# Kernel optimization log

Hardware: AMD Instinct MI355X
Metric: run time of the kernel (lower is better)

Reference implementation:

```python
import jax, jax.numpy as jnp
import numpy as np

# torch.rrelu in eval mode uses slope = (lower+upper)/2 = (1/8 + 1/3)/2
RRELU_SLOPE = (1.0 / 8.0 + 1.0 / 3.0) / 2.0

N_NODES = 50000
N_EDGES = 800000
EMB_FEATS = 128
IN_FEATS = 128
HIDDEN = 64


def setup_inputs() -> dict:
    key = jax.random.key(0)
    ks = jax.random.split(key, 16)
    z = jax.random.normal(ks[0], (N_NODES, EMB_FEATS), dtype=jnp.float32)
    x = jax.random.normal(ks[1], (N_NODES, IN_FEATS), dtype=jnp.float32)
    edge_index = jax.random.randint(ks[2], (2, N_EDGES), 0, N_NODES, dtype=jnp.int32)

    def glorot(k, shape):
        fan_in, fan_out = shape
        lim = jnp.sqrt(6.0 / (fan_in + fan_out))
        return jax.random.uniform(k, shape, jnp.float32, -lim, lim)

    return {
        "z": z,
        "x": x,
        "edge_index": edge_index,
        "W_e1": glorot(ks[3], (EMB_FEATS, HIDDEN)),
        "b_e1": jnp.zeros((HIDDEN,), jnp.float32),
        "W_e2": glorot(ks[4], (HIDDEN, HIDDEN)),
        "b_e2": jnp.zeros((HIDDEN,), jnp.float32),
        "W_f1": glorot(ks[5], (IN_FEATS, HIDDEN)),
        "b_f1": jnp.zeros((HIDDEN,), jnp.float32),
        "W_f2": glorot(ks[6], (HIDDEN, HIDDEN)),
        "b_f2": jnp.zeros((HIDDEN,), jnp.float32),
        "W_out": glorot(ks[7], (HIDDEN, 1)),
        "b_out": jnp.zeros((1,), jnp.float32),
    }


def gcn_conv(h_in, W, b, src, dst, n_nodes):
    """PyG GCNConv: self-loops + symmetric deg^-1/2 normalization."""
    h = h_in @ W  # [N, out]
    # degree of self-loop-augmented graph: indeg + 1
    indeg = jax.ops.segment_sum(
        jnp.ones(dst.shape[0], h.dtype), dst, num_segments=n_nodes)
    deg = indeg + 1.0
    dinv = jnp.where(deg > 0, 1.0 / jnp.sqrt(deg), 0.0)  # [N]
    norm = dinv[src] * dinv[dst]  # [E]
    # neighbor messages (gather + scatter-add)
    agg = jax.ops.segment_sum(h[src] * norm[:, None], dst, num_segments=n_nodes)
    # self-loop contribution: dinv[i]*dinv[i]*h[i]
    agg = agg + h * (dinv * dinv)[:, None]
    return agg + b


def _rrelu(t):
    return jnp.where(t >= 0, t, t * RRELU_SLOPE)


def reference(z, x, edge_index, W_e1, b_e1, W_e2, b_e2,
              W_f1, b_f1, W_f2, b_f2, W_out, b_out):
    src, dst = edge_index[0], edge_index[1]
    n = z.shape[0]
    ze = _rrelu(gcn_conv(z, W_e1, b_e1, src, dst, n))
    ze = jnp.tanh(gcn_conv(ze, W_e2, b_e2, src, dst, n))
    xf = _rrelu(gcn_conv(x, W_f1, b_f1, src, dst, n))
    xf = jnp.tanh(gcn_conv(xf, W_f2, b_f2, src, dst, n))
    return (ze * xf) @ W_out + b_out  # [N, 1]
```

## Files before the change

### kernel.cpp

```cpp
#include <hip/hip_runtime.h>
#include <hip/hip_fp16.h>
#include <math.h>

#define RRELU_SLOPE 0.22916667f


__global__ __launch_bounds__(256) void k_deg(const int* __restrict__ dst, int E,
                                             int* __restrict__ cnt) {
    int e = blockIdx.x * 256 + threadIdx.x;
    if (e < E) atomicAdd(&cnt[dst[e]], 1);
}

__global__ __launch_bounds__(256) void k_scan1(const int* __restrict__ cnt, int N,
                                               int* __restrict__ bsum) {
    int i = blockIdx.x * 256 + threadIdx.x;
    int v = (i < N) ? cnt[i] : 0;
    for (int o = 32; o >= 1; o >>= 1) v += __shfl_xor(v, o, 64);
    __shared__ int ws[4];
    if ((threadIdx.x & 63) == 0) ws[threadIdx.x >> 6] = v;
    __syncthreads();
    if (threadIdx.x == 0) bsum[blockIdx.x] = ws[0] + ws[1] + ws[2] + ws[3];
}

__global__ __launch_bounds__(256) void k_scan2(const int* __restrict__ bsum, int NB,
                                               int* __restrict__ boff,
                                               int* __restrict__ rowp, int N, int E) {
    __shared__ int s[256];
    int t = threadIdx.x;
    int v[4];
    int loc = 0;
    for (int i = 0; i < 4; i++) {
        int idx = t * 4 + i;
        v[i] = (idx < NB) ? bsum[idx] : 0;
        loc += v[i];
    }
    s[t] = loc;
    __syncthreads();
    for (int o = 1; o < 256; o <<= 1) {
        int u = (t >= o) ? s[t - o] : 0;
        __syncthreads();
        s[t] += u;
        __syncthreads();
    }
    int excl = s[t] - loc;
    for (int i = 0; i < 4; i++) {
        int idx = t * 4 + i;
        if (idx < NB) { boff[idx] = excl; excl += v[i]; }
    }
    if (t == 0) rowp[N] = E;
}

__global__ __launch_bounds__(256) void k_scan3(const int* __restrict__ cnt,
                                               const int* __restrict__ boff, int N,
                                               int* __restrict__ rowp,
                                               int* __restrict__ nxt,
                                               float* __restrict__ dinv) {
    int i = blockIdx.x * 256 + threadIdx.x;
    int lane = threadIdx.x & 63, wid = threadIdx.x >> 6;
    int v = (i < N) ? cnt[i] : 0;
    int inc = v;
    for (int o = 1; o < 64; o <<= 1) {
        int u = __shfl_up(inc, o, 64);
        if (lane >= o) inc += u;
    }
    __shared__ int wsum[4];
    if (lane == 63) wsum[wid] = inc;
    __syncthreads();
    int wo = 0;
    for (int w = 0; w < wid; w++) wo += wsum[w];
    if (i < N) {
        int excl = inc - v + wo + boff[blockIdx.x];
        rowp[i] = excl;
        nxt[i] = excl;
        dinv[i] = 1.0f / sqrtf((float)v + 1.0f);
    }
}

__global__ __launch_bounds__(256) void k_fill(const int* __restrict__ src,
                                              const int* __restrict__ dst, int E,
                                              int* __restrict__ nxt,
                                              const float* __restrict__ dinv,
                                              int2* __restrict__ pair) {
    int e = blockIdx.x * 256 + threadIdx.x;
    if (e >= E) return;
    int s = src[e], d = dst[e];
    int p = atomicAdd(&nxt[d], 1);
    float v = dinv[s] * dinv[d];
    pair[p] = make_int2(s, __float_as_int(v));
}

__global__ __launch_bounds__(256) void k_mm1(const float* __restrict__ Zin,
                                             const float* __restrict__ Xin,
                                             const float* __restrict__ Wz,
                                             const float* __restrict__ Wx,
                                             __half2* __restrict__ H, int N) {
    __shared__ float Asz[64][20], Asx[64][20];
    __shared__ float Wsz[16][64], Wsx[16][64];
    const int tid = threadIdx.x;
    const int tc = tid & 15, tr = tid >> 4;
    const int row0 = blockIdx.x * 64;
    const int srow = tid >> 2, sk = (tid & 3) * 4;
    const int wk = tid >> 4, wc = (tid & 15) * 4;

    float cz[4][4] = {}, cx[4][4] = {};

    for (int k0 = 0; k0 < 128; k0 += 16) {
        float4 a0 = make_float4(0.f, 0.f, 0.f, 0.f);
        float4 a1 = make_float4(0.f, 0.f, 0.f, 0.f);
        int gr = row0 + srow;
        if (gr < N) {
            a0 = *(const float4*)(Zin + (size_t)gr * 128 + k0 + sk);
            a1 = *(const float4*)(Xin + (size_t)gr * 128 + k0 + sk);
        }
        float4 w0 = *(const float4*)(Wz + (size_t)(k0 + wk) * 64 + wc);
        float4 w1 = *(const float4*)(Wx + (size_t)(k0 + wk) * 64 + wc);
        __syncthreads();
        *(float4*)&Asz[srow][sk] = a0;
        *(float4*)&Asx[srow][sk] = a1;
        *(float4*)&Wsz[wk][wc] = w0;
        *(float4*)&Wsx[wk][wc] = w1;
        __syncthreads();

#pragma unroll
        for (int k = 0; k < 16; k += 4) {
            float4 vz[4], vx[4];
#pragma unroll
            for (int i = 0; i < 4; i++) {
                vz[i] = *(const float4*)&Asz[tr * 4 + i][k];
                vx[i] = *(const float4*)&Asx[tr * 4 + i][k];
            }
#pragma unroll
            for (int kk = 0; kk < 4; kk++) {
                float4 wzv = *(const float4*)&Wsz[k + kk][tc * 4];
                float4 wxv = *(const float4*)&Wsx[k + kk][tc * 4];
#pragma unroll
                for (int i = 0; i < 4; i++) {
                    float a = ((const float*)&vz[i])[kk];
                    float b = ((const float*)&vx[i])[kk];
                    cz[i][0] = fmaf(a, wzv.x, cz[i][0]);
                    cz[i][1] = fmaf(a, wzv.y, cz[i][1]);
                    cz[i][2] = fmaf(a, wzv.z, cz[i][2]);
                    cz[i][3] = fmaf(a, wzv.w, cz[i][3]);
                    cx[i][0] = fmaf(b, wxv.x, cx[i][0]);
                    cx[i][1] = fmaf(b, wxv.y, cx[i][1]);
                    cx[i][2] = fmaf(b, wxv.z, cx[i][2]);
                    cx[i][3] = fmaf(b, wxv.w, cx[i][3]);
                }
            }
        }
    }

#pragma unroll
    for (int i = 0; i < 4; i++) {
        int r = row0 + tr * 4 + i;
        if (r < N) {
            union { __half2 h[4]; float4 f; } u;
#pragma unroll
            for (int j = 0; j < 4; j++) u.h[j] = __floats2half2_rn(cz[i][j], cx[i][j]);
            *(float4*)(H + (size_t)r * 64 + tc * 4) = u.f;
        }
    }
}

__global__ __launch_bounds__(256) void k_mm2i(const float* __restrict__ Azx,
                                              const float* __restrict__ Wz,
                                              const float* __restrict__ Wx,
                                              __half2* __restrict__ H, int N) {
    __shared__ float As[64][36];
    __shared__ float Wsz[16][64], Wsx[16][64];
    const int tid = threadIdx.x;
    const int tc = tid & 15, tr = tid >> 4;
    const int row0 = blockIdx.x * 64;
    const int srow = tid >> 2, soff = (tid & 3) * 8;
    const int wk = tid >> 4, wc = (tid & 15) * 4;

    float cz[4][4] = {}, cx[4][4] = {};

    for (int k0 = 0; k0 < 64; k0 += 16) {
        float4 a0 = make_float4(0.f, 0.f, 0.f, 0.f);
        float4 a1 = make_float4(0.f, 0.f, 0.f, 0.f);
        int gr = row0 + srow;
        if (gr < N) {
            a0 = *(const float4*)(Azx + (size_t)gr * 128 + 2 * k0 + soff);
            a1 = *(const float4*)(Azx + (size_t)gr * 128 + 2 * k0 + soff + 4);
        }
        float4 w0 = *(const float4*)(Wz + (size_t)(k0 + wk) * 64 + wc);
        float4 w1 = *(const float4*)(Wx + (size_t)(k0 + wk) * 64 + wc);
        __syncthreads();
        *(float4*)&As[srow][soff] = a0;
        *(float4*)&As[srow][soff + 4] = a1;
        *(float4*)&Wsz[wk][wc] = w0;
        *(float4*)&Wsx[wk][wc] = w1;
        __syncthreads();

#pragma unroll
        for (int k = 0; k < 16; k += 2) {
            float4 v[4];
#pragma unroll
            for (int i = 0; i < 4; i++) v[i] = *(const float4*)&As[tr * 4 + i][2 * k];
#pragma unroll
            for (int kk = 0; kk < 2; kk++) {
                float4 wzv = *(const float4*)&Wsz[k + kk][tc * 4];
                float4 wxv = *(const float4*)&Wsx[k + kk][tc * 4];
#pragma unroll
                for (int i = 0; i < 4; i++) {
                    float a = kk ? v[i].z : v[i].x;
                    float b = kk ? v[i].w : v[i].y;
                    cz[i][0] = fmaf(a, wzv.x, cz[i][0]);
                    cz[i][1] = fmaf(a, wzv.y, cz[i][1]);
                    cz[i][2] = fmaf(a, wzv.z, cz[i][2]);
                    cz[i][3] = fmaf(a, wzv.w, cz[i][3]);
                    cx[i][0] = fmaf(b, wxv.x, cx[i][0]);
                    cx[i][1] = fmaf(b, wxv.y, cx[i][1]);
                    cx[i][2] = fmaf(b, wxv.z, cx[i][2]);
                    cx[i][3] = fmaf(b, wxv.w, cx[i][3]);
                }
            }
        }
    }

#pragma unroll
    for (int i = 0; i < 4; i++) {
        int r = row0 + tr * 4 + i;
        if (r < N) {
            union { __half2 h[4]; float4 f; } u;
#pragma unroll
            for (int j = 0; j < 4; j++) u.h[j] = __floats2half2_rn(cz[i][j], cx[i][j]);
            *(float4*)(H + (size_t)r * 64 + tc * 4) = u.f;
        }
    }
}

__global__ __launch_bounds__(256) void k_agg_act(
    const int* __restrict__ rowp, const int2* __restrict__ pair,
    const float* __restrict__ dinv, const __half2* __restrict__ H,
    const float* __restrict__ bz, const float* __restrict__ bx,
    float* __restrict__ A, int N) {
    int wid = threadIdx.x >> 6, lane = threadIdx.x & 63;
    int i = blockIdx.x * 4 + wid;
    if (i >= N) return;
    int beg = rowp[i], end = rowp[i + 1];
    float2 s0 = {0.f, 0.f}, s1 = {0.f, 0.f}, s2 = {0.f, 0.f}, s3 = {0.f, 0.f};
    int p = beg;
    if (p < end && (p & 1)) {
        int2 cv = pair[p++];
        float2 h = __half22float2(H[(size_t)cv.x * 64 + lane]);
        float w = __int_as_float(cv.y);
        s0.x = fmaf(w, h.x, s0.x);
        s0.y = fmaf(w, h.y, s0.y);
    }
    for (; p + 8 <= end; p += 8) {
        int4 pa = *(const int4*)(pair + p);
        int4 pb = *(const int4*)(pair + p + 2);
        int4 pc = *(const int4*)(pair + p + 4);
        int4 pd = *(const int4*)(pair + p + 6);
        float2 h0 = __half22float2(H[(size_t)pa.x * 64 + lane]);
        float2 h1 = __half22float2(H[(size_t)pa.z * 64 + lane]);
        float2 h2 = __half22float2(H[(size_t)pb.x * 64 + lane]);
        float2 h3 = __half22float2(H[(size_t)pb.z * 64 + lane]);
        float2 h4 = __half22float2(H[(size_t)pc.x * 64 + lane]);
        float2 h5 = __half22float2(H[(size_t)pc.z * 64 + lane]);
        float2 h6 = __half22float2(H[(size_t)pd.x * 64 + lane]);
        float2 h7 = __half22float2(H[(size_t)pd.z * 64 + lane]);
        float w0 = __int_as_float(pa.y), w1 = __int_as_float(pa.w);
        float w2 = __int_as_float(pb.y), w3 = __int_as_float(pb.w);
        float w4 = __int_as_float(pc.y), w5 = __int_as_float(pc.w);
        float w6 = __int_as_float(pd.y), w7 = __int_as_float(pd.w);
        s0.x = fmaf(w0, h0.x, s0.x); s0.y = fmaf(w0, h0.y, s0.y);
        s1.x = fmaf(w1, h1.x, s1.x); s1.y = fmaf(w1, h1.y, s1.y);
        s2.x = fmaf(w2, h2.x, s2.x); s2.y = fmaf(w2, h2.y, s2.y);
        s3.x = fmaf(w3, h3.x, s3.x); s3.y = fmaf(w3, h3.y, s3.y);
        s0.x = fmaf(w4, h4.x, s0.x); s0.y = fmaf(w4, h4.y, s0.y);
        s1.x = fmaf(w5, h5.x, s1.x); s1.y = fmaf(w5, h5.y, s1.y);
        s2.x = fmaf(w6, h6.x, s2.x); s2.y = fmaf(w6, h6.y, s2.y);
        s3.x = fmaf(w7, h7.x, s3.x); s3.y = fmaf(w7, h7.y, s3.y);
    }
    for (; p + 2 <= end; p += 2) {
        int4 pa = *(const int4*)(pair + p);
        float2 h0 = __half22float2(H[(size_t)pa.x * 64 + lane]);
        float2 h1 = __half22float2(H[(size_t)pa.z * 64 + lane]);
        float w0 = __int_as_float(pa.y), w1 = __int_as_float(pa.w);
        s0.x = fmaf(w0, h0.x, s0.x); s0.y = fmaf(w0, h0.y, s0.y);
        s1.x = fmaf(w1, h1.x, s1.x); s1.y = fmaf(w1, h1.y, s1.y);
    }
    if (p < end) {
        int2 cv = pair[p];
        float2 h = __half22float2(H[(size_t)cv.x * 64 + lane]);
        float w = __int_as_float(cv.y);
        s0.x = fmaf(w, h.x, s0.x);
        s0.y = fmaf(w, h.y, s0.y);
    }
    float sz = (s0.x + s1.x) + (s2.x + s3.x);
    float sx = (s0.y + s1.y) + (s2.y + s3.y);
    float dv = dinv[i], sw = dv * dv;
    float2 hs = __half22float2(H[(size_t)i * 64 + lane]);
    sz = fmaf(sw, hs.x, sz) + bz[lane];
    sx = fmaf(sw, hs.y, sx) + bx[lane];
    sz = sz >= 0.f ? sz : sz * RRELU_SLOPE;
    sx = sx >= 0.f ? sx : sx * RRELU_SLOPE;
    *((float2*)(A + (size_t)i * 128) + lane) = make_float2(sz, sx);
}

__global__ __launch_bounds__(256) void k_agg_final(
    const int* __restrict__ rowp, const int2* __restrict__ pair,
    const float* __restrict__ dinv, const __half2* __restrict__ H,
    const float* __restrict__ bz, const float* __restrict__ bx,
    const float* __restrict__ Wout, const float* __restrict__ bout,
    float* __restrict__ out, int N) {
    int wid = threadIdx.x >> 6, lane = threadIdx.x & 63;
    int i = blockIdx.x * 4 + wid;
    if (i >= N) return;
    int beg = rowp[i], end = rowp[i + 1];
    float2 s0 = {0.f, 0.f}, s1 = {0.f, 0.f}, s2 = {0.f, 0.f}, s3 = {0.f, 0.f};
    int p = beg;
    if (p < end && (p & 1)) {
        int2 cv = pair[p++];
        float2 h = __half22float2(H[(size_t)cv.x * 64 + lane]);
        float w = __int_as_float(cv.y);
        s0.x = fmaf(w, h.x, s0.x);
        s0.y = fmaf(w, h.y, s0.y);
    }
    for (; p + 8 <= end; p += 8) {
        int4 pa = *(const int4*)(pair + p);
        int4 pb = *(const int4*)(pair + p + 2);
        int4 pc = *(const int4*)(pair + p + 4);
        int4 pd = *(const int4*)(pair + p + 6);
        float2 h0 = __half22float2(H[(size_t)pa.x * 64 + lane]);
        float2 h1 = __half22float2(H[(size_t)pa.z * 64 + lane]);
        float2 h2 = __half22float2(H[(size_t)pb.x * 64 + lane]);
        float2 h3 = __half22float2(H[(size_t)pb.z * 64 + lane]);
        float2 h4 = __half22float2(H[(size_t)pc.x * 64 + lane]);
        float2 h5 = __half22float2(H[(size_t)pc.z * 64 + lane]);
        float2 h6 = __half22float2(H[(size_t)pd.x * 64 + lane]);
        float2 h7 = __half22float2(H[(size_t)pd.z * 64 + lane]);
        float w0 = __int_as_float(pa.y), w1 = __int_as_float(pa.w);
        float w2 = __int_as_float(pb.y), w3 = __int_as_float(pb.w);
        float w4 = __int_as_float(pc.y), w5 = __int_as_float(pc.w);
        float w6 = __int_as_float(pd.y), w7 = __int_as_float(pd.w);
        s0.x = fmaf(w0, h0.x, s0.x); s0.y = fmaf(w0, h0.y, s0.y);
        s1.x = fmaf(w1, h1.x, s1.x); s1.y = fmaf(w1, h1.y, s1.y);
        s2.x = fmaf(w2, h2.x, s2.x); s2.y = fmaf(w2, h2.y, s2.y);
        s3.x = fmaf(w3, h3.x, s3.x); s3.y = fmaf(w3, h3.y, s3.y);
        s0.x = fmaf(w4, h4.x, s0.x); s0.y = fmaf(w4, h4.y, s0.y);
        s1.x = fmaf(w5, h5.x, s1.x); s1.y = fmaf(w5, h5.y, s1.y);
        s2.x = fmaf(w6, h6.x, s2.x); s2.y = fmaf(w6, h6.y, s2.y);
        s3.x = fmaf(w7, h7.x, s3.x); s3.y = fmaf(w7, h7.y, s3.y);
    }
    for (; p + 2 <= end; p += 2) {
        int4 pa = *(const int4*)(pair + p);
        float2 h0 = __half22float2(H[(size_t)pa.x * 64 + lane]);
        float2 h1 = __half22float2(H[(size_t)pa.z * 64 + lane]);
        float w0 = __int_as_float(pa.y), w1 = __int_as_float(pa.w);
        s0.x = fmaf(w0, h0.x, s0.x); s0.y = fmaf(w0, h0.y, s0.y);
        s1.x = fmaf(w1, h1.x, s1.x); s1.y = fmaf(w1, h1.y, s1.y);
    }
    if (p < end) {
        int2 cv = pair[p];
        float2 h = __half22float2(H[(size_t)cv.x * 64 + lane]);
        float w = __int_as_float(cv.y);
        s0.x = fmaf(w, h.x, s0.x);
        s0.y = fmaf(w, h.y, s0.y);
    }
    float sz = (s0.x + s1.x) + (s2.x + s3.x);
    float sx = (s0.y + s1.y) + (s2.y + s3.y);
    float dv = dinv[i], sw = dv * dv;
    float2 hs = __half22float2(H[(size_t)i * 64 + lane]);
    sz = fmaf(sw, hs.x, sz) + bz[lane];
    sx = fmaf(sw, hs.y, sx) + bx[lane];
    float prod = tanhf(sz) * tanhf(sx) * Wout[lane];
    for (int o = 32; o >= 1; o >>= 1) prod += __shfl_xor(prod, o, 64);
    if (lane == 0) out[i] = prod + bout[0];
}


extern "C" void kernel_launch(void* const* d_in, const int* in_sizes, int n_in,
                              void* d_out, int out_size, void* d_ws, size_t ws_size,
                              hipStream_t stream) {
    const float* z = (const float*)d_in[0];
    const float* x = (const float*)d_in[1];
    const int* ei = (const int*)d_in[2];
    const float* We1 = (const float*)d_in[3];
    const float* be1 = (const float*)d_in[4];
    const float* We2 = (const float*)d_in[5];
    const float* be2 = (const float*)d_in[6];
    const float* Wf1 = (const float*)d_in[7];
    const float* bf1 = (const float*)d_in[8];
    const float* Wf2 = (const float*)d_in[9];
    const float* bf2 = (const float*)d_in[10];
    const float* Wout = (const float*)d_in[11];
    const float* bout = (const float*)d_in[12];
    float* out = (float*)d_out;

    int N = in_sizes[0] / 128;
    int E = in_sizes[2] / 2;
    const int* src = ei;
    const int* dst = ei + E;

    char* base = (char*)d_ws;
    size_t off = 0;
    auto take = [&](size_t nbytes) -> char* {
        char* p = base + off;
        off = (off + nbytes + 255) & ~(size_t)255;
        return p;
    };
    int NB = (N + 255) / 256;
    int* cnt = (int*)take((size_t)N * 4);
    int* bsum = (int*)take(1024 * 4);
    int* boff = (int*)take(1024 * 4);
    int* rowp = (int*)take(((size_t)N + 1) * 4);
    int* nxt = (int*)take((size_t)N * 4);
    float* dinv = (float*)take((size_t)N * 4);
    int2* pair = (int2*)take((size_t)E * 8);
    __half2* hzx = (__half2*)take((size_t)N * 64 * 4);
    float* azx = (float*)take((size_t)N * 128 * 4);

    hipMemsetAsync(cnt, 0, (size_t)N * 4, stream);

    int egrid = (E + 255) / 256;
    k_deg<<<egrid, 256, 0, stream>>>(dst, E, cnt);
    k_scan1<<<NB, 256, 0, stream>>>(cnt, N, bsum);
    k_scan2<<<1, 256, 0, stream>>>(bsum, NB, boff, rowp, N, E);
    k_scan3<<<NB, 256, 0, stream>>>(cnt, boff, N, rowp, nxt, dinv);
    k_fill<<<egrid, 256, 0, stream>>>(src, dst, E, nxt, dinv, pair);

    int mmgrid = (N + 63) / 64;
    int agrid = (N + 3) / 4;

    k_mm1<<<mmgrid, 256, 0, stream>>>(z, x, We1, Wf1, hzx, N);
    k_agg_act<<<agrid, 256, 0, stream>>>(rowp, pair, dinv, hzx, be1, bf1, azx, N);
    k_mm2i<<<mmgrid, 256, 0, stream>>>(azx, We2, Wf2, hzx, N);
    k_agg_final<<<agrid, 256, 0, stream>>>(rowp, pair, dinv, hzx, be2, bf2, Wout,
                                           bout, out, N);
}
```

Before: 227.2 us.

## Build CSR from atomic ranks and recompute edge weights from dinv in aggregation

The degree-count kernel now records each edge's atomic rank, so the fill kernel places source indices directly at rowp[dst]+rank with no second atomic pass. The CSR stores only source indices (4 bytes per edge) instead of (src, weight) pairs, and the aggregation kernels recompute each edge weight as dinv[src]*dinv[dst] on the fly. This removes the second round of atomics and halves edge-list traffic in both aggregation passes. In exchange it adds a per-edge rank array and an extra random dinv gather per edge in each aggregation.

```diff
diff --git a/kernel.cpp b/kernel.cpp
--- a/kernel.cpp
+++ b/kernel.cpp
@@ -6,9 +6,10 @@
 
 
 __global__ __launch_bounds__(256) void k_deg(const int* __restrict__ dst, int E,
-                                             int* __restrict__ cnt) {
+                                             int* __restrict__ cnt,
+                                             int* __restrict__ rank) {
     int e = blockIdx.x * 256 + threadIdx.x;
-    if (e < E) atomicAdd(&cnt[dst[e]], 1);
+    if (e < E) rank[e] = atomicAdd(&cnt[dst[e]], 1);
 }
 
 __global__ __launch_bounds__(256) void k_scan1(const int* __restrict__ cnt, int N,
@@ -53,7 +54,6 @@
 __global__ __launch_bounds__(256) void k_scan3(const int* __restrict__ cnt,
                                                const int* __restrict__ boff, int N,
                                                int* __restrict__ rowp,
-                                               int* __restrict__ nxt,
                                                float* __restrict__ dinv) {
     int i = blockIdx.x * 256 + threadIdx.x;
     int lane = threadIdx.x & 63, wid = threadIdx.x >> 6;
@@ -71,22 +71,19 @@
     if (i < N) {
         int excl = inc - v + wo + boff[blockIdx.x];
         rowp[i] = excl;
-        nxt[i] = excl;
         dinv[i] = 1.0f / sqrtf((float)v + 1.0f);
     }
 }
 
 __global__ __launch_bounds__(256) void k_fill(const int* __restrict__ src,
-                                              const int* __restrict__ dst, int E,
-                                              int* __restrict__ nxt,
-                                              const float* __restrict__ dinv,
-                                              int2* __restrict__ pair) {
+                                              const int* __restrict__ dst,
+                                              const int* __restrict__ rank, int E,
+                                              const int* __restrict__ rowp,
+                                              int* __restrict__ csrc) {
     int e = blockIdx.x * 256 + threadIdx.x;
     if (e >= E) return;
-    int s = src[e], d = dst[e];
-    int p = atomicAdd(&nxt[d], 1);
-    float v = dinv[s] * dinv[d];
-    pair[p] = make_int2(s, __float_as_int(v));
+    int d = dst[e];
+    csrc[rowp[d] + rank[e]] = src[e];
 }
 
 __global__ __launch_bounds__(256) void k_mm1(const float* __restrict__ Zin,
@@ -231,8 +228,16 @@
     }
 }
 
+#define AGG_EDGE(S, C)                                            \
+    {                                                             \
+        float2 h_ = __half22float2(H[(size_t)(C)*64 + lane]);     \
+        float w_ = dinv[C] * dvi;                                 \
+        S.x = fmaf(w_, h_.x, S.x);                                \
+        S.y = fmaf(w_, h_.y, S.y);                                \
+    }
+
 __global__ __launch_bounds__(256) void k_agg_act(
-    const int* __restrict__ rowp, const int2* __restrict__ pair,
+    const int* __restrict__ rowp, const int* __restrict__ csrc,
     const float* __restrict__ dinv, const __half2* __restrict__ H,
     const float* __restrict__ bz, const float* __restrict__ bx,
     float* __restrict__ A, int N) {
@@ -240,59 +245,40 @@
     int i = blockIdx.x * 4 + wid;
     if (i >= N) return;
     int beg = rowp[i], end = rowp[i + 1];
+    float dvi = dinv[i];
     float2 s0 = {0.f, 0.f}, s1 = {0.f, 0.f}, s2 = {0.f, 0.f}, s3 = {0.f, 0.f};
     int p = beg;
-    if (p < end && (p & 1)) {
-        int2 cv = pair[p++];
-        float2 h = __half22float2(H[(size_t)cv.x * 64 + lane]);
-        float w = __int_as_float(cv.y);
-        s0.x = fmaf(w, h.x, s0.x);
-        s0.y = fmaf(w, h.y, s0.y);
+    while (p < end && (p & 3)) {
+        int c = csrc[p++];
+        AGG_EDGE(s0, c);
     }
     for (; p + 8 <= end; p += 8) {
-        int4 pa = *(const int4*)(pair + p);
-        int4 pb = *(const int4*)(pair + p + 2);
-        int4 pc = *(const int4*)(pair + p + 4);
-        int4 pd = *(const int4*)(pair + p + 6);
-        float2 h0 = __half22float2(H[(size_t)pa.x * 64 + lane]);
-        float2 h1 = __half22float2(H[(size_t)pa.z * 64 + lane]);
-        float2 h2 = __half22float2(H[(size_t)pb.x * 64 + lane]);
-        float2 h3 = __half22float2(H[(size_t)pb.z * 64 + lane]);
-        float2 h4 = __half22float2(H[(size_t)pc.x * 64 + lane]);
-        float2 h5 = __half22float2(H[(size_t)pc.z * 64 + lane]);
-        float2 h6 = __half22float2(H[(size_t)pd.x * 64 + lane]);
-        float2 h7 = __half22float2(H[(size_t)pd.z * 64 + lane]);
-        float w0 = __int_as_float(pa.y), w1 = __int_as_float(pa.w);
-        float w2 = __int_as_float(pb.y), w3 = __int_as_float(pb.w);
-        float w4 = __int_as_float(pc.y), w5 = __int_as_float(pc.w);
-        float w6 = __int_as_float(pd.y), w7 = __int_as_float(pd.w);
-        s0.x = fmaf(w0, h0.x, s0.x); s0.y = fmaf(w0, h0.y, s0.y);
-        s1.x = fmaf(w1, h1.x, s1.x); s1.y = fmaf(w1, h1.y, s1.y);
-        s2.x = fmaf(w2, h2.x, s2.x); s2.y = fmaf(w2, h2.y, s2.y);
-        s3.x = fmaf(w3, h3.x, s3.x); s3.y = fmaf(w3, h3.y, s3.y);
-        s0.x = fmaf(w4, h4.x, s0.x); s0.y = fmaf(w4, h4.y, s0.y);
-        s1.x = fmaf(w5, h5.x, s1.x); s1.y = fmaf(w5, h5.y, s1.y);
-        s2.x = fmaf(w6, h6.x, s2.x); s2.y = fmaf(w6, h6.y, s2.y);
-        s3.x = fmaf(w7, h7.x, s3.x); s3.y = fmaf(w7, h7.y, s3.y);
-    }
-    for (; p + 2 <= end; p += 2) {
-        int4 pa = *(const int4*)(pair + p);
-        float2 h0 = __half22float2(H[(size_t)pa.x * 64 + lane]);
-        float2 h1 = __half22float2(H[(size_t)pa.z * 64 + lane]);
-        float w0 = __int_as_float(pa.y), w1 = __int_as_float(pa.w);
-        s0.x = fmaf(w0, h0.x, s0.x); s0.y = fmaf(w0, h0.y, s0.y);
-        s1.x = fmaf(w1, h1.x, s1.x); s1.y = fmaf(w1, h1.y, s1.y);
-    }
-    if (p < end) {
-        int2 cv = pair[p];
-        float2 h = __half22float2(H[(size_t)cv.x * 64 + lane]);
-        float w = __int_as_float(cv.y);
-        s0.x = fmaf(w, h.x, s0.x);
-        s0.y = fmaf(w, h.y, s0.y);
+        int4 ca = *(const int4*)(csrc + p);
+        int4 cb = *(const int4*)(csrc + p + 4);
+        AGG_EDGE(s0, ca.x);
+        AGG_EDGE(s1, ca.y);
+        AGG_EDGE(s2, ca.z);
+        AGG_EDGE(s3, ca.w);
+        AGG_EDGE(s0, cb.x);
+        AGG_EDGE(s1, cb.y);
+        AGG_EDGE(s2, cb.z);
+        AGG_EDGE(s3, cb.w);
+    }
+    if (p + 4 <= end) {
+        int4 ca = *(const int4*)(csrc + p);
+        AGG_EDGE(s0, ca.x);
+        AGG_EDGE(s1, ca.y);
+        AGG_EDGE(s2, ca.z);
+        AGG_EDGE(s3, ca.w);
+        p += 4;
+    }
+    while (p < end) {
+        int c = csrc[p++];
+        AGG_EDGE(s0, c);
     }
     float sz = (s0.x + s1.x) + (s2.x + s3.x);
     float sx = (s0.y + s1.y) + (s2.y + s3.y);
-    float dv = dinv[i], sw = dv * dv;
+    float sw = dvi * dvi;
     float2 hs = __half22float2(H[(size_t)i * 64 + lane]);
     sz = fmaf(sw, hs.x, sz) + bz[lane];
     sx = fmaf(sw, hs.y, sx) + bx[lane];
@@ -302,7 +288,7 @@
 }
 
 __global__ __launch_bounds__(256) void k_agg_final(
-    const int* __restrict__ rowp, const int2* __restrict__ pair,
+    const int* __restrict__ rowp, const int* __restrict__ csrc,
     const float* __restrict__ dinv, const __half2* __restrict__ H,
     const float* __restrict__ bz, const float* __restrict__ bx,
     const float* __restrict__ Wout, const float* __restrict__ bout,
@@ -311,59 +297,40 @@
     int i = blockIdx.x * 4 + wid;
     if (i >= N) return;
     int beg = rowp[i], end = rowp[i + 1];
+    float dvi = dinv[i];
     float2 s0 = {0.f, 0.f}, s1 = {0.f, 0.f}, s2 = {0.f, 0.f}, s3 = {0.f, 0.f};
     int p = beg;
-    if (p < end && (p & 1)) {
-        int2 cv = pair[p++];
-        float2 h = __half22float2(H[(size_t)cv.x * 64 + lane]);
-        float w = __int_as_float(cv.y);
-        s0.x = fmaf(w, h.x, s0.x);
-        s0.y = fmaf(w, h.y, s0.y);
+    while (p < end && (p & 3)) {
+        int c = csrc[p++];
+        AGG_EDGE(s0, c);
     }
     for (; p + 8 <= end; p += 8) {
-        int4 pa = *(const int4*)(pair + p);
-        int4 pb = *(const int4*)(pair + p + 2);
-        int4 pc = *(const int4*)(pair + p + 4);
-        int4 pd = *(const int4*)(pair + p + 6);
-        float2 h0 = __half22float2(H[(size_t)pa.x * 64 + lane]);
-        float2 h1 = __half22float2(H[(size_t)pa.z * 64 + lane]);
-        float2 h2 = __half22float2(H[(size_t)pb.x * 64 + lane]);
-        float2 h3 = __half22float2(H[(size_t)pb.z * 64 + lane]);
-        float2 h4 = __half22float2(H[(size_t)pc.x * 64 + lane]);
-        float2 h5 = __half22float2(H[(size_t)pc.z * 64 + lane]);
-        float2 h6 = __half22float2(H[(size_t)pd.x * 64 + lane]);
-        float2 h7 = __half22float2(H[(size_t)pd.z * 64 + lane]);
-        float w0 = __int_as_float(pa.y), w1 = __int_as_float(pa.w);
-        float w2 = __int_as_float(pb.y), w3 = __int_as_float(pb.w);
-        float w4 = __int_as_float(pc.y), w5 = __int_as_float(pc.w);
-        float w6 = __int_as_float(pd.y), w7 = __int_as_float(pd.w);
-        s0.x = fmaf(w0, h0.x, s0.x); s0.y = fmaf(w0, h0.y, s0.y);
-        s1.x = fmaf(w1, h1.x, s1.x); s1.y = fmaf(w1, h1.y, s1.y);
-        s2.x = fmaf(w2, h2.x, s2.x); s2.y = fmaf(w2, h2.y, s2.y);
-        s3.x = fmaf(w3, h3.x, s3.x); s3.y = fmaf(w3, h3.y, s3.y);
-        s0.x = fmaf(w4, h4.x, s0.x); s0.y = fmaf(w4, h4.y, s0.y);
-        s1.x = fmaf(w5, h5.x, s1.x); s1.y = fmaf(w5, h5.y, s1.y);
-        s2.x = fmaf(w6, h6.x, s2.x); s2.y = fmaf(w6, h6.y, s2.y);
-        s3.x = fmaf(w7, h7.x, s3.x); s3.y = fmaf(w7, h7.y, s3.y);
-    }
-    for (; p + 2 <= end; p += 2) {
-        int4 pa = *(const int4*)(pair + p);
-        float2 h0 = __half22float2(H[(size_t)pa.x * 64 + lane]);
-        float2 h1 = __half22float2(H[(size_t)pa.z * 64 + lane]);
-        float w0 = __int_as_float(pa.y), w1 = __int_as_float(pa.w);
-        s0.x = fmaf(w0, h0.x, s0.x); s0.y = fmaf(w0, h0.y, s0.y);
-        s1.x = fmaf(w1, h1.x, s1.x); s1.y = fmaf(w1, h1.y, s1.y);
-    }
-    if (p < end) {
-        int2 cv = pair[p];
-        float2 h = __half22float2(H[(size_t)cv.x * 64 + lane]);
-        float w = __int_as_float(cv.y);
-        s0.x = fmaf(w, h.x, s0.x);
-        s0.y = fmaf(w, h.y, s0.y);
+        int4 ca = *(const int4*)(csrc + p);
+        int4 cb = *(const int4*)(csrc + p + 4);
+        AGG_EDGE(s0, ca.x);
+        AGG_EDGE(s1, ca.y);
+        AGG_EDGE(s2, ca.z);
+        AGG_EDGE(s3, ca.w);
+        AGG_EDGE(s0, cb.x);
+        AGG_EDGE(s1, cb.y);
+        AGG_EDGE(s2, cb.z);
+        AGG_EDGE(s3, cb.w);
+    }
+    if (p + 4 <= end) {
+        int4 ca = *(const int4*)(csrc + p);
+        AGG_EDGE(s0, ca.x);
+        AGG_EDGE(s1, ca.y);
+        AGG_EDGE(s2, ca.z);
+        AGG_EDGE(s3, ca.w);
+        p += 4;
+    }
+    while (p < end) {
+        int c = csrc[p++];
+        AGG_EDGE(s0, c);
     }
     float sz = (s0.x + s1.x) + (s2.x + s3.x);
     float sx = (s0.y + s1.y) + (s2.y + s3.y);
-    float dv = dinv[i], sw = dv * dv;
+    float sw = dvi * dvi;
     float2 hs = __half22float2(H[(size_t)i * 64 + lane]);
     sz = fmaf(sw, hs.x, sz) + bz[lane];
     sx = fmaf(sw, hs.y, sx) + bx[lane];
@@ -408,27 +375,27 @@
     int* bsum = (int*)take(1024 * 4);
     int* boff = (int*)take(1024 * 4);
     int* rowp = (int*)take(((size_t)N + 1) * 4);
-    int* nxt = (int*)take((size_t)N * 4);
     float* dinv = (float*)take((size_t)N * 4);
-    int2* pair = (int2*)take((size_t)E * 8);
+    int* rank = (int*)take((size_t)E * 4);
+    int* csrc = (int*)take((size_t)E * 4);
     __half2* hzx = (__half2*)take((size_t)N * 64 * 4);
     float* azx = (float*)take((size_t)N * 128 * 4);
 
     hipMemsetAsync(cnt, 0, (size_t)N * 4, stream);
 
     int egrid = (E + 255) / 256;
-    k_deg<<<egrid, 256, 0, stream>>>(dst, E, cnt);
+    k_deg<<<egrid, 256, 0, stream>>>(dst, E, cnt, rank);
     k_scan1<<<NB, 256, 0, stream>>>(cnt, N, bsum);
     k_scan2<<<1, 256, 0, stream>>>(bsum, NB, boff, rowp, N, E);
-    k_scan3<<<NB, 256, 0, stream>>>(cnt, boff, N, rowp, nxt, dinv);
-    k_fill<<<egrid, 256, 0, stream>>>(src, dst, E, nxt, dinv, pair);
+    k_scan3<<<NB, 256, 0, stream>>>(cnt, boff, N, rowp, dinv);
+    k_fill<<<egrid, 256, 0, stream>>>(src, dst, rank, E, rowp, csrc);
 
     int mmgrid = (N + 63) / 64;
     int agrid = (N + 3) / 4;
 
     k_mm1<<<mmgrid, 256, 0, stream>>>(z, x, We1, Wf1, hzx, N);
-    k_agg_act<<<agrid, 256, 0, stream>>>(rowp, pair, dinv, hzx, be1, bf1, azx, N);
+    k_agg_act<<<agrid, 256, 0, stream>>>(rowp, csrc, dinv, hzx, be1, bf1, azx, N);
     k_mm2i<<<mmgrid, 256, 0, stream>>>(azx, We2, Wf2, hzx, N);
-    k_agg_final<<<agrid, 256, 0, stream>>>(rowp, pair, dinv, hzx, be2, bf2, Wout,
+    k_agg_final<<<agrid, 256, 0, stream>>>(rowp, csrc, dinv, hzx, be2, bf2, Wout,
                                            bout, out, N);
 }
```

New measurement: 203.5 us. -10.4%, faster.
